# Kernel optimization log

Hardware: AMD Instinct MI355X
Metric: run time of the kernel (lower is better)

Reference implementation:

```python
import jax, jax.numpy as jnp
import numpy as np

# Flax nn.LSTMCell math: gates i,f,g,o; input dense has no bias, hidden dense has bias.
# We fuse the four gate projections into single [D,4H] / [H,4H] matrices in order (i,f,g,o).

def _lstm_layer(x, Wx, Wh, b):
    # x: [B,T,D], Wx: [D,4H], Wh: [H,4H], b: [4H]
    B = x.shape[0]
    H = Wh.shape[0]
    # Precompute input projections for the whole sequence (one big GEMM).
    xW = jnp.einsum('btd,dg->btg', x, Wx) + b  # [B,T,4H]

    def step(carry, xw_t):
        c, h = carry
        z = xw_t + h @ Wh  # [B,4H]
        i, f, g, o = jnp.split(z, 4, axis=-1)
        i = jax.nn.sigmoid(i)
        f = jax.nn.sigmoid(f)
        g = jnp.tanh(g)
        o = jax.nn.sigmoid(o)
        c = f * c + i * g
        h = o * jnp.tanh(c)
        return (c, h), h

    init = (jnp.zeros((B, H), x.dtype), jnp.zeros((B, H), x.dtype))
    _, ys = jax.lax.scan(step, init, jnp.swapaxes(xW, 0, 1))  # scan over T
    return jnp.swapaxes(ys, 0, 1)  # [B,T,H]


def setup_inputs() -> dict:
    key = jax.random.key(0)
    ks = jax.random.split(key, 7)
    B, T, D, H = 64, 512, 512, 1024
    s = lambda fan_in: 1.0 / np.sqrt(fan_in)
    x = jax.random.normal(ks[0], (B, T, D), dtype=jnp.float32)
    Wx0 = jax.random.normal(ks[1], (D, 4 * H), dtype=jnp.float32) * s(D)
    Wh0 = jax.random.normal(ks[2], (H, 4 * H), dtype=jnp.float32) * s(H)
    b0 = jnp.zeros((4 * H,), dtype=jnp.float32)
    Wx1 = jax.random.normal(ks[3], (H, 4 * H), dtype=jnp.float32) * s(H)
    Wh1 = jax.random.normal(ks[4], (H, 4 * H), dtype=jnp.float32) * s(H)
    b1 = jnp.zeros((4 * H,), dtype=jnp.float32)
    return {"x": x, "Wx0": Wx0, "Wh0": Wh0, "b0": b0, "Wx1": Wx1, "Wh1": Wh1, "b1": b1}


def reference(x, Wx0, Wh0, b0, Wx1, Wh1, b1):
    h1 = _lstm_layer(x, Wx0, Wh0, b0)
    h2 = _lstm_layer(h1, Wx1, Wh1, b1)
    return h2
```

## Files before the change

kernel.cpp:

```cpp
#include <hip/hip_runtime.h>

typedef __attribute__((ext_vector_type(8))) short short8;
typedef __attribute__((ext_vector_type(4))) float f32x4;

#define WS_XB     0ull
#define WS_W0T    33554432ull
#define WS_W1T    46137344ull
#define WS_RING0  62914560ull
#define WS_RING1  67108864ull
#define WS_BAR    71303168ull
#define SLOT_ELEMS 65536
#define SLOT_BYTES 131072

#define BAR_ARR(g)  ((g) * 16)
#define BAR_ROOT    256
#define BAR_REL(g)  (272 + (g) * 16)

__device__ __forceinline__ unsigned short f2bf(float f) {
  unsigned u = __float_as_uint(f);
  u += 0x7FFFu + ((u >> 16) & 1u);
  return (unsigned short)(u >> 16);
}

__device__ __forceinline__ float sigm(float x) { return 1.0f / (1.0f + __expf(-x)); }

__global__ void sentinel_kernel(float* out) { out[0] = 1.0e6f; }

__global__ void convert_x_kernel(const float* __restrict__ x, unsigned short* __restrict__ xb) {
  int i = blockIdx.x * 256 + threadIdx.x;
  const float4 v = ((const float4*)x)[i];
  unsigned long long pack = (unsigned long long)f2bf(v.x)
                          | ((unsigned long long)f2bf(v.y) << 16)
                          | ((unsigned long long)f2bf(v.z) << 32)
                          | ((unsigned long long)f2bf(v.w) << 48);
  ((unsigned long long*)xb)[i] = pack;
}

__global__ void transpose_weights_kernel(const float* __restrict__ wx, const float* __restrict__ wh,
                                         unsigned short* __restrict__ dst, int Kx, int Ktot) {
  __shared__ float tile[32][33];
  const int k0 = blockIdx.x * 32, n0 = blockIdx.y * 32;
  const int tx = threadIdx.x, ty = threadIdx.y;
#pragma unroll
  for (int i = 0; i < 4; ++i) {
    int k = k0 + ty + i * 8;
    tile[ty + i * 8][tx] = (k < Kx) ? wx[(size_t)k * 4096 + n0 + tx]
                                    : wh[(size_t)(k - Kx) * 4096 + n0 + tx];
  }
  __syncthreads();
#pragma unroll
  for (int i = 0; i < 4; ++i) {
    int n = n0 + ty + i * 8;
    int r = (n & 1023) * 4 + (n >> 10);
    dst[(size_t)r * Ktot + k0 + tx] = f2bf(tile[tx][ty + i * 8]);
  }
}

template<int N1, int NBLK>
__device__ __forceinline__ void lstm_step_mfma(int a0b, int a1b,
    const unsigned short* __restrict__ r1p, const unsigned short* __restrict__ r2p,
    f32x4& acc0, f32x4& acc1)
{
  extern __shared__ unsigned short lds[];
  short8 buf[4][8];

  auto loadB = [&](int slot, int blk) {
    const unsigned short* p = (blk < N1) ? (r1p + blk * 256) : (r2p + (blk - N1) * 256);
#pragma unroll
    for (int j = 0; j < 8; ++j) buf[slot][j] = *(const short8*)(p + j * 32);
  };
  auto compute8 = [&](int slot, int kg) {
#pragma unroll
    for (int j = 0; j < 8; ++j) {
      const int ko = kg + j * 32;
      short8 a0 = *(const short8*)&lds[a0b + ko];
      short8 a1 = *(const short8*)&lds[a1b + ko];
      acc0 = __builtin_amdgcn_mfma_f32_16x16x32_bf16(a0, buf[slot][j], acc0, 0, 0, 0);
      acc1 = __builtin_amdgcn_mfma_f32_16x16x32_bf16(a1, buf[slot][j], acc1, 0, 0, 0);
    }
  };

  loadB(0, 0); loadB(1, 1); loadB(2, 2); loadB(3, 3);
  __builtin_amdgcn_sched_barrier(0);
#pragma unroll
  for (int bp = 0; bp < NBLK; ++bp) {
    compute8(bp & 3, bp * 256);
    if (bp + 4 < NBLK) loadB(bp & 3, bp + 4);
    __builtin_amdgcn_sched_barrier(0);
  }
}

__global__ void __launch_bounds__(256, 1) lstm_persistent(
    const unsigned short* __restrict__ xb,
    const unsigned short* __restrict__ w0t,
    const unsigned short* __restrict__ w1t,
    const float* __restrict__ b0v, const float* __restrict__ b1v,
    unsigned short* __restrict__ ring0, unsigned short* __restrict__ ring1,
    unsigned* __restrict__ bar,
    float* __restrict__ out)
{
  extern __shared__ unsigned short lds[];

  const int wg    = blockIdx.x;
  const int group = wg >> 7;
  const int wgl   = wg & 127;
  const int hu0   = wgl * 8;
  const int tid   = threadIdx.x;
  const int lane  = tid & 63;
  const int wid   = tid >> 6;
  const int c16   = lane & 15;
  const int row4  = lane >> 4;
  const int bb    = wid * 16 + c16;

  const int K    = group ? 2048 : 1536;
  const int KPAD = group ? 2056 : 1544;

  {
    const unsigned short* wsrc = (group ? w1t : w0t) + (size_t)(wgl * 32) * K;
    const int kv = K >> 3;
    for (int c = tid; c < 32 * kv; c += 256) {
      int r = c / kv, q = c - r * kv;
      int srcr = 8 * ((r & 15) >> 2) + 4 * (r >> 4) + (r & 3);
      *(short8*)&lds[r * KPAD + q * 8] = *(const short8*)&wsrc[(size_t)srcr * K + q * 8];
    }
  }
  __syncthreads();

  const float* bsrc = group ? b1v : b0v;
  float bias0[4], bias1[4];
#pragma unroll
  for (int j = 0; j < 4; ++j) {
    bias0[j] = bsrc[j * 1024 + hu0 + 2 * row4];
    bias1[j] = bsrc[j * 1024 + hu0 + 2 * row4 + 1];
  }

  const int a0b = c16 * KPAD + 8 * row4;
  const int a1b = a0b + 16 * KPAD;

  const int lofs = (bb << 10) + 8 * row4;
  const unsigned short* x_cur = xb + ((size_t)bb << 18) + 8 * row4;
  unsigned* rwb = (unsigned*)(group ? ring1 : ring0) + (((bb << 10) + hu0) >> 1) + row4;
  float* out_base = out + ((size_t)bb << 19) + hu0 + 2 * row4;

  const int mygrp = wg >> 4;
  unsigned* grpc  = bar + BAR_ARR(mygrp);
  unsigned* rootc = bar + BAR_ROOT;
  unsigned* relc  = bar + BAR_REL(mygrp);

  float cst0 = 0.0f, cst1 = 0.0f;

  for (int s = 0; s <= 512; ++s) {
    const bool active = group ? (s >= 1) : (s < 512);
    if (active) {
      const int t = group ? (s - 1) : s;

      f32x4 acc0 = { bias0[0], bias0[1], bias0[2], bias0[3] };
      f32x4 acc1 = { bias1[0], bias1[1], bias1[2], bias1[3] };

      const unsigned short* h0rd = ring0 + ((s - 1) & 31) * SLOT_ELEMS + lofs;
      if (group == 0) {
        lstm_step_mfma<2, 6>(a0b, a1b, x_cur, h0rd, acc0, acc1);
        x_cur += 512;
      } else {
        const unsigned short* h1rd = ring1 + ((s - 2) & 31) * SLOT_ELEMS + lofs;
        lstm_step_mfma<4, 8>(a0b, a1b, h0rd, h1rd, acc0, acc1);
      }

      float hv0, hv1;
      {
        float iv = sigm(acc0[0]), fv = sigm(acc0[1]);
        float gv = tanhf(acc0[2]), ov = sigm(acc0[3]);
        cst0 = fv * cst0 + iv * gv;
        hv0 = ov * tanhf(cst0);
      }
      {
        float iv = sigm(acc1[0]), fv = sigm(acc1[1]);
        float gv = tanhf(acc1[2]), ov = sigm(acc1[3]);
        cst1 = fv * cst1 + iv * gv;
        hv1 = ov * tanhf(cst1);
      }
      unsigned hp = (unsigned)f2bf(hv0) | ((unsigned)f2bf(hv1) << 16);
      (void)__hip_atomic_exchange(rwb + (t & 31) * (SLOT_ELEMS / 2), hp,
                                  __ATOMIC_RELAXED, __HIP_MEMORY_SCOPE_AGENT);
      if (group) {
        float2 o2; o2.x = hv0; o2.y = hv1;
        *(float2*)(out_base + ((size_t)t << 10)) = o2;
      }
    }

    __syncthreads();
    if (tid == 0) {
      unsigned old = __hip_atomic_fetch_add(grpc, 1u, __ATOMIC_RELAXED, __HIP_MEMORY_SCOPE_AGENT);
      if (old == (unsigned)(16 * s + 15)) {
        unsigned old2 = __hip_atomic_fetch_add(rootc, 1u, __ATOMIC_RELAXED, __HIP_MEMORY_SCOPE_AGENT);
        if (old2 == (unsigned)(16 * s + 15)) {
#pragma unroll
          for (int g2 = 0; g2 < 16; ++g2)
            (void)__hip_atomic_exchange(bar + BAR_REL(g2), (unsigned)(s + 1),
                                        __ATOMIC_RELAXED, __HIP_MEMORY_SCOPE_AGENT);
        }
      }
      while (__hip_atomic_load(relc, __ATOMIC_RELAXED, __HIP_MEMORY_SCOPE_AGENT) < (unsigned)(s + 1))
        __builtin_amdgcn_s_sleep(1);
    }
    __syncthreads();
  }
}

extern "C" void kernel_launch(void* const* d_in, const int* in_sizes, int n_in,
                              void* d_out, int out_size, void* d_ws, size_t ws_size,
                              hipStream_t stream) {
  const float* x   = (const float*)d_in[0];
  const float* Wx0 = (const float*)d_in[1];
  const float* Wh0 = (const float*)d_in[2];
  const float* b0  = (const float*)d_in[3];
  const float* Wx1 = (const float*)d_in[4];
  const float* Wh1 = (const float*)d_in[5];
  const float* b1  = (const float*)d_in[6];
  float* outp = (float*)d_out;

  char* ws = (char*)d_ws;
  unsigned short* xbp   = (unsigned short*)(ws + WS_XB);
  unsigned short* w0tp  = (unsigned short*)(ws + WS_W0T);
  unsigned short* w1tp  = (unsigned short*)(ws + WS_W1T);
  unsigned short* ring0 = (unsigned short*)(ws + WS_RING0);
  unsigned short* ring1 = (unsigned short*)(ws + WS_RING1);
  unsigned*       barp  = (unsigned*)(ws + WS_BAR);

  sentinel_kernel<<<dim3(1), dim3(1), 0, stream>>>(outp);
  convert_x_kernel<<<dim3(16384), dim3(256), 0, stream>>>(x, xbp);
  transpose_weights_kernel<<<dim3(48, 128), dim3(32, 8), 0, stream>>>(Wx0, Wh0, w0tp, 512, 1536);
  transpose_weights_kernel<<<dim3(64, 128), dim3(32, 8), 0, stream>>>(Wx1, Wh1, w1tp, 1024, 2048);
  hipMemsetAsync(ring0 + 31 * SLOT_ELEMS, 0, SLOT_BYTES, stream);
  hipMemsetAsync(ring1 + 31 * SLOT_ELEMS, 0, SLOT_BYTES, stream);
  hipMemsetAsync(barp, 0, 4096, stream);

  void* kargs[] = { (void*)&xbp, (void*)&w0tp, (void*)&w1tp, (void*)&b0, (void*)&b1,
                    (void*)&ring0, (void*)&ring1, (void*)&barp, (void*)&outp };
  hipError_t e = hipLaunchCooperativeKernel((void*)lstm_persistent, dim3(256), dim3(256),
                                            kargs, 32 * 2056 * 2 , stream);
  if (e != hipSuccess) {
    lstm_persistent<<<dim3(256), dim3(256), 32 * 2056 * 2, stream>>>(
        xbp, w0tp, w1tp, b0, b1, ring0, ring1, barp, outp);
  }
}
```

Measured before the change: 5.195 ms.

## Replace hierarchical grid barrier with flat per-group counters and decoupled layer progress

Replaces the two-level arrive/root/release grid barrier with 16 flat per-group arrival counters that a whole wavefront polls at once with a ballot. Layer-0 blocks now wait only on layer-0 peers for the current step, plus a loose check that layer 1 is no more than about 30 steps behind so the ring is not overrun; layer-1 blocks wait on all groups. This removes the serialized release hop and lets layer 0 run ahead of layer 1. It also preloads all B fragments for a step into registers at once instead of a 4-deep rotating buffer, and shrinks the LDS row padding to 2 elements, which makes 16-byte LDS reads misaligned and may raise bank conflicts or register pressure.

```diff
diff --git a/kernel.cpp b/kernel.cpp
--- a/kernel.cpp
+++ b/kernel.cpp
@@ -12,10 +12,6 @@
 #define SLOT_ELEMS 65536
 #define SLOT_BYTES 131072
 
-#define BAR_ARR(g)  ((g) * 16)
-#define BAR_ROOT    256
-#define BAR_REL(g)  (272 + (g) * 16)
-
 __device__ __forceinline__ unsigned short f2bf(float f) {
   unsigned u = __float_as_uint(f);
   u += 0x7FFFu + ((u >> 16) & 1u);
@@ -62,31 +58,30 @@
     f32x4& acc0, f32x4& acc1)
 {
   extern __shared__ unsigned short lds[];
-  short8 buf[4][8];
-
-  auto loadB = [&](int slot, int blk) {
-    const unsigned short* p = (blk < N1) ? (r1p + blk * 256) : (r2p + (blk - N1) * 256);
-#pragma unroll
-    for (int j = 0; j < 8; ++j) buf[slot][j] = *(const short8*)(p + j * 32);
-  };
-  auto compute8 = [&](int slot, int kg) {
+  short8 buf[NBLK][8];
+
+#pragma unroll
+  for (int bp = 0; bp < NBLK; ++bp) {
+    const unsigned short* p = (bp < N1) ? (r1p + bp * 256) : (r2p + (bp - N1) * 256);
+#pragma unroll
+    for (int j = 0; j < 8; ++j) buf[bp][j] = *(const short8*)(p + j * 32);
+  }
+  __builtin_amdgcn_sched_barrier(0);
+
+#pragma unroll
+  for (int bp = 0; bp < NBLK; ++bp) {
+#pragma unroll
+    for (int j = 0; j < 8; ++j)
+      asm volatile("" :: "v"(buf[bp][j]));
+    __builtin_amdgcn_sched_barrier(0);
 #pragma unroll
     for (int j = 0; j < 8; ++j) {
-      const int ko = kg + j * 32;
+      const int ko = bp * 256 + j * 32;
       short8 a0 = *(const short8*)&lds[a0b + ko];
       short8 a1 = *(const short8*)&lds[a1b + ko];
-      acc0 = __builtin_amdgcn_mfma_f32_16x16x32_bf16(a0, buf[slot][j], acc0, 0, 0, 0);
-      acc1 = __builtin_amdgcn_mfma_f32_16x16x32_bf16(a1, buf[slot][j], acc1, 0, 0, 0);
-    }
-  };
-
-  loadB(0, 0); loadB(1, 1); loadB(2, 2); loadB(3, 3);
-  __builtin_amdgcn_sched_barrier(0);
-#pragma unroll
-  for (int bp = 0; bp < NBLK; ++bp) {
-    compute8(bp & 3, bp * 256);
-    if (bp + 4 < NBLK) loadB(bp & 3, bp + 4);
-    __builtin_amdgcn_sched_barrier(0);
+      acc0 = __builtin_amdgcn_mfma_f32_16x16x32_bf16(a0, buf[bp][j], acc0, 0, 0, 0);
+      acc1 = __builtin_amdgcn_mfma_f32_16x16x32_bf16(a1, buf[bp][j], acc1, 0, 0, 0);
+    }
   }
 }
 
@@ -113,7 +108,7 @@
   const int bb    = wid * 16 + c16;
 
   const int K    = group ? 2048 : 1536;
-  const int KPAD = group ? 2056 : 1544;
+  const int KPAD = group ? 2050 : 1538;
 
   {
     const unsigned short* wsrc = (group ? w1t : w0t) + (size_t)(wgl * 32) * K;
@@ -142,69 +137,70 @@
   unsigned* rwb = (unsigned*)(group ? ring1 : ring0) + (((bb << 10) + hu0) >> 1) + row4;
   float* out_base = out + ((size_t)bb << 19) + hu0 + 2 * row4;
 
-  const int mygrp = wg >> 4;
-  unsigned* grpc  = bar + BAR_ARR(mygrp);
-  unsigned* rootc = bar + BAR_ROOT;
-  unsigned* relc  = bar + BAR_REL(mygrp);
-
   float cst0 = 0.0f, cst1 = 0.0f;
 
-  for (int s = 0; s <= 512; ++s) {
-    const bool active = group ? (s >= 1) : (s < 512);
-    if (active) {
-      const int t = group ? (s - 1) : s;
-
-      f32x4 acc0 = { bias0[0], bias0[1], bias0[2], bias0[3] };
-      f32x4 acc1 = { bias1[0], bias1[1], bias1[2], bias1[3] };
-
-      const unsigned short* h0rd = ring0 + ((s - 1) & 31) * SLOT_ELEMS + lofs;
-      if (group == 0) {
-        lstm_step_mfma<2, 6>(a0b, a1b, x_cur, h0rd, acc0, acc1);
-        x_cur += 512;
-      } else {
-        const unsigned short* h1rd = ring1 + ((s - 2) & 31) * SLOT_ELEMS + lofs;
-        lstm_step_mfma<4, 8>(a0b, a1b, h0rd, h1rd, acc0, acc1);
-      }
-
-      float hv0, hv1;
-      {
-        float iv = sigm(acc0[0]), fv = sigm(acc0[1]);
-        float gv = tanhf(acc0[2]), ov = sigm(acc0[3]);
-        cst0 = fv * cst0 + iv * gv;
-        hv0 = ov * tanhf(cst0);
-      }
-      {
-        float iv = sigm(acc1[0]), fv = sigm(acc1[1]);
-        float gv = tanhf(acc1[2]), ov = sigm(acc1[3]);
-        cst1 = fv * cst1 + iv * gv;
-        hv1 = ov * tanhf(cst1);
-      }
-      unsigned hp = (unsigned)f2bf(hv0) | ((unsigned)f2bf(hv1) << 16);
-      (void)__hip_atomic_exchange(rwb + (t & 31) * (SLOT_ELEMS / 2), hp,
-                                  __ATOMIC_RELAXED, __HIP_MEMORY_SCOPE_AGENT);
-      if (group) {
-        float2 o2; o2.x = hv0; o2.y = hv1;
-        *(float2*)(out_base + ((size_t)t << 10)) = o2;
-      }
-    }
+  auto compute_episode = [&](int s) {
+    const int t = group ? (s - 1) : s;
+
+    f32x4 acc0 = { bias0[0], bias0[1], bias0[2], bias0[3] };
+    f32x4 acc1 = { bias1[0], bias1[1], bias1[2], bias1[3] };
+
+    const unsigned short* h0rd = ring0 + ((s - 1) & 31) * SLOT_ELEMS + lofs;
+    if (group == 0) {
+      lstm_step_mfma<2, 6>(a0b, a1b, x_cur, h0rd, acc0, acc1);
+      x_cur += 512;
+    } else {
+      const unsigned short* h1rd = ring1 + ((s - 2) & 31) * SLOT_ELEMS + lofs;
+      lstm_step_mfma<4, 8>(a0b, a1b, h0rd, h1rd, acc0, acc1);
+    }
+
+    float hv0, hv1;
+    {
+      float iv = sigm(acc0[0]), fv = sigm(acc0[1]);
+      float gv = tanhf(acc0[2]), ov = sigm(acc0[3]);
+      cst0 = fv * cst0 + iv * gv;
+      hv0 = ov * tanhf(cst0);
+    }
+    {
+      float iv = sigm(acc1[0]), fv = sigm(acc1[1]);
+      float gv = tanhf(acc1[2]), ov = sigm(acc1[3]);
+      cst1 = fv * cst1 + iv * gv;
+      hv1 = ov * tanhf(cst1);
+    }
+    unsigned hp = (unsigned)f2bf(hv0) | ((unsigned)f2bf(hv1) << 16);
+    (void)__hip_atomic_exchange(rwb + (t & 31) * (SLOT_ELEMS / 2), hp,
+                                __ATOMIC_RELAXED, __HIP_MEMORY_SCOPE_AGENT);
+    if (group) {
+      float2 o2; o2.x = hv0; o2.y = hv1;
+      *(float2*)(out_base + ((size_t)t << 10)) = o2;
+    }
+  };
+
+  for (int s = 0; s < 512; ++s) {
+    const bool active = group ? (s >= 1) : true;
+    if (active) compute_episode(s);
 
     __syncthreads();
-    if (tid == 0) {
-      unsigned old = __hip_atomic_fetch_add(grpc, 1u, __ATOMIC_RELAXED, __HIP_MEMORY_SCOPE_AGENT);
-      if (old == (unsigned)(16 * s + 15)) {
-        unsigned old2 = __hip_atomic_fetch_add(rootc, 1u, __ATOMIC_RELAXED, __HIP_MEMORY_SCOPE_AGENT);
-        if (old2 == (unsigned)(16 * s + 15)) {
-#pragma unroll
-          for (int g2 = 0; g2 < 16; ++g2)
-            (void)__hip_atomic_exchange(bar + BAR_REL(g2), (unsigned)(s + 1),
-                                        __ATOMIC_RELAXED, __HIP_MEMORY_SCOPE_AGENT);
+    if (wid == 0) {
+      if (lane == 0)
+        __hip_atomic_fetch_add(bar + (wg >> 4), 1u, __ATOMIC_RELAXED, __HIP_MEMORY_SCOPE_AGENT);
+      const bool last = (group == 0) && (s == 511);
+      if (!last) {
+        int tgt;
+        if (group == 0) tgt = (lane < 8) ? 16 * (s + 1) : 16 * (s - 29);
+        else            tgt = 16 * (s + 1);
+        for (;;) {
+          int v = (lane < 16)
+            ? (int)__hip_atomic_load(bar + lane, __ATOMIC_RELAXED, __HIP_MEMORY_SCOPE_AGENT)
+            : 0x7FFFFFFF;
+          if (__ballot(v >= tgt) == ~0ull) break;
+          __builtin_amdgcn_s_sleep(1);
         }
       }
-      while (__hip_atomic_load(relc, __ATOMIC_RELAXED, __HIP_MEMORY_SCOPE_AGENT) < (unsigned)(s + 1))
-        __builtin_amdgcn_s_sleep(1);
     }
     __syncthreads();
   }
+  if (group) compute_episode(512);
 }
 
 extern "C" void kernel_launch(void* const* d_in, const int* in_sizes, int n_in,
@@ -238,9 +234,9 @@
   void* kargs[] = { (void*)&xbp, (void*)&w0tp, (void*)&w1tp, (void*)&b0, (void*)&b1,
                     (void*)&ring0, (void*)&ring1, (void*)&barp, (void*)&outp };
   hipError_t e = hipLaunchCooperativeKernel((void*)lstm_persistent, dim3(256), dim3(256),
-                                            kargs, 32 * 2056 * 2 , stream);
+                                            kargs, 32 * 2050 * 2 , stream);
   if (e != hipSuccess) {
-    lstm_persistent<<<dim3(256), dim3(256), 32 * 2056 * 2, stream>>>(
+    lstm_persistent<<<dim3(256), dim3(256), 32 * 2050 * 2, stream>>>(
         xbp, w0tp, w1tp, b0, b1, ring0, ring1, barp, outp);
   }
 }
```

Measured after the change: 10.89 ms. 2.1x slower.

## Flatten grid barrier to single counter, unroll B prefetch, shrink LDS padding

Applied to the files above, without the earlier changes.

Replaces the two-level (group then root) atomic barrier with a single global counter that all 256 workgroups increment, after which the last arriver writes release flags for the 16 groups. This removes one serialized atomic round-trip per step at the cost of more contention on a single address. It also manually unrolls the 4-slot B-register prefetch pipeline into named arrays so the per-slot indexing is static. It changes the LDS row padding from 8 to 2 elements, which alters the bank-conflict pattern of the weight reads.

```diff
diff --git a/kernel.cpp b/kernel.cpp
--- a/kernel.cpp
+++ b/kernel.cpp
@@ -12,10 +12,6 @@
 #define SLOT_ELEMS 65536
 #define SLOT_BYTES 131072
 
-#define BAR_ARR(g)  ((g) * 16)
-#define BAR_ROOT    256
-#define BAR_REL(g)  (272 + (g) * 16)
-
 __device__ __forceinline__ unsigned short f2bf(float f) {
   unsigned u = __float_as_uint(f);
   u += 0x7FFFu + ((u >> 16) & 1u);
@@ -62,32 +58,35 @@
     f32x4& acc0, f32x4& acc1)
 {
   extern __shared__ unsigned short lds[];
-  short8 buf[4][8];
-
-  auto loadB = [&](int slot, int blk) {
-    const unsigned short* p = (blk < N1) ? (r1p + blk * 256) : (r2p + (blk - N1) * 256);
-#pragma unroll
-    for (int j = 0; j < 8; ++j) buf[slot][j] = *(const short8*)(p + j * 32);
+  short8 s0[8], s1[8], s2[8], s3[8];
+
+  auto ldp = [&](int blk) { return (blk < N1) ? (r1p + blk * 256) : (r2p + (blk - N1) * 256); };
+  auto issue = [&](short8* dst, int blk) {
+    const unsigned short* p = ldp(blk);
+#pragma unroll
+    for (int j = 0; j < 8; ++j) dst[j] = *(const short8*)(p + j * 32);
   };
-  auto compute8 = [&](int slot, int kg) {
+  auto compute8 = [&](const short8* b, int bp) {
 #pragma unroll
     for (int j = 0; j < 8; ++j) {
-      const int ko = kg + j * 32;
+      const int ko = bp * 256 + j * 32;
       short8 a0 = *(const short8*)&lds[a0b + ko];
       short8 a1 = *(const short8*)&lds[a1b + ko];
-      acc0 = __builtin_amdgcn_mfma_f32_16x16x32_bf16(a0, buf[slot][j], acc0, 0, 0, 0);
-      acc1 = __builtin_amdgcn_mfma_f32_16x16x32_bf16(a1, buf[slot][j], acc1, 0, 0, 0);
+      acc0 = __builtin_amdgcn_mfma_f32_16x16x32_bf16(a0, b[j], acc0, 0, 0, 0);
+      acc1 = __builtin_amdgcn_mfma_f32_16x16x32_bf16(a1, b[j], acc1, 0, 0, 0);
     }
   };
 
-  loadB(0, 0); loadB(1, 1); loadB(2, 2); loadB(3, 3);
+  issue(s0, 0); issue(s1, 1); issue(s2, 2); issue(s3, 3);
   __builtin_amdgcn_sched_barrier(0);
-#pragma unroll
-  for (int bp = 0; bp < NBLK; ++bp) {
-    compute8(bp & 3, bp * 256);
-    if (bp + 4 < NBLK) loadB(bp & 3, bp + 4);
-    __builtin_amdgcn_sched_barrier(0);
-  }
+  compute8(s0, 0); if (NBLK > 4) { issue(s0, 4); __builtin_amdgcn_sched_barrier(0); }
+  compute8(s1, 1); if (NBLK > 5) { issue(s1, 5); __builtin_amdgcn_sched_barrier(0); }
+  compute8(s2, 2); if (NBLK > 6) { issue(s2, 6); __builtin_amdgcn_sched_barrier(0); }
+  compute8(s3, 3); if (NBLK > 7) { issue(s3, 7); __builtin_amdgcn_sched_barrier(0); }
+  if (NBLK > 4) compute8(s0, 4);
+  if (NBLK > 5) compute8(s1, 5);
+  if (NBLK > 6) compute8(s2, 6);
+  if (NBLK > 7) compute8(s3, 7);
 }
 
 __global__ void __launch_bounds__(256, 1) lstm_persistent(
@@ -113,7 +112,7 @@
   const int bb    = wid * 16 + c16;
 
   const int K    = group ? 2048 : 1536;
-  const int KPAD = group ? 2056 : 1544;
+  const int KPAD = group ? 2050 : 1538;
 
   {
     const unsigned short* wsrc = (group ? w1t : w0t) + (size_t)(wgl * 32) * K;
@@ -142,10 +141,8 @@
   unsigned* rwb = (unsigned*)(group ? ring1 : ring0) + (((bb << 10) + hu0) >> 1) + row4;
   float* out_base = out + ((size_t)bb << 19) + hu0 + 2 * row4;
 
-  const int mygrp = wg >> 4;
-  unsigned* grpc  = bar + BAR_ARR(mygrp);
-  unsigned* rootc = bar + BAR_ROOT;
-  unsigned* relc  = bar + BAR_REL(mygrp);
+  unsigned* rootc = bar;
+  unsigned* relc  = bar + 16 + (wg >> 4) * 16;
 
   float cst0 = 0.0f, cst1 = 0.0f;
 
@@ -190,15 +187,12 @@
 
     __syncthreads();
     if (tid == 0) {
-      unsigned old = __hip_atomic_fetch_add(grpc, 1u, __ATOMIC_RELAXED, __HIP_MEMORY_SCOPE_AGENT);
-      if (old == (unsigned)(16 * s + 15)) {
-        unsigned old2 = __hip_atomic_fetch_add(rootc, 1u, __ATOMIC_RELAXED, __HIP_MEMORY_SCOPE_AGENT);
-        if (old2 == (unsigned)(16 * s + 15)) {
-#pragma unroll
-          for (int g2 = 0; g2 < 16; ++g2)
-            (void)__hip_atomic_exchange(bar + BAR_REL(g2), (unsigned)(s + 1),
-                                        __ATOMIC_RELAXED, __HIP_MEMORY_SCOPE_AGENT);
-        }
+      unsigned old = __hip_atomic_fetch_add(rootc, 1u, __ATOMIC_RELAXED, __HIP_MEMORY_SCOPE_AGENT);
+      if (old == 256u * (unsigned)(s + 1) - 1u) {
+#pragma unroll
+        for (int g2 = 0; g2 < 16; ++g2)
+          (void)__hip_atomic_exchange(bar + 16 + g2 * 16, (unsigned)(s + 1),
+                                      __ATOMIC_RELAXED, __HIP_MEMORY_SCOPE_AGENT);
       }
       while (__hip_atomic_load(relc, __ATOMIC_RELAXED, __HIP_MEMORY_SCOPE_AGENT) < (unsigned)(s + 1))
         __builtin_amdgcn_s_sleep(1);
@@ -238,9 +232,9 @@
   void* kargs[] = { (void*)&xbp, (void*)&w0tp, (void*)&w1tp, (void*)&b0, (void*)&b1,
                     (void*)&ring0, (void*)&ring1, (void*)&barp, (void*)&outp };
   hipError_t e = hipLaunchCooperativeKernel((void*)lstm_persistent, dim3(256), dim3(256),
-                                            kargs, 32 * 2056 * 2 , stream);
+                                            kargs, 32 * 2050 * 2 , stream);
   if (e != hipSuccess) {
-    lstm_persistent<<<dim3(256), dim3(256), 32 * 2056 * 2, stream>>>(
+    lstm_persistent<<<dim3(256), dim3(256), 32 * 2050 * 2, stream>>>(
         xbp, w0tp, w1tp, b0, b1, ring0, ring1, barp, outp);
   }
 }
```

Result: slower. 10.31 ms (+98.5%).

## Split grid barrier per layer with cross-layer mirror flags and packed h stores

Applied to the files above, without the earlier changes.

Replaces the single 256-workgroup barrier with two per-layer barriers (8 sub-groups each). Each layer also waits on a mirror flag from the other layer: layer 0 may run up to 16 steps ahead of layer 1 within the 32-slot ring, while layer 1 waits for layer 0's current step. This is meant to decouple the layers and shorten the critical path of each barrier. It also packs two lanes' hidden outputs into one 64-bit atomic store via a shuffle and drops the sched_barriers in the MFMA loop. The risks are ring-slot reuse hazards and visibility ordering, since all atomics are relaxed.

```diff
diff --git a/kernel.cpp b/kernel.cpp
--- a/kernel.cpp
+++ b/kernel.cpp
@@ -12,9 +12,14 @@
 #define SLOT_ELEMS 65536
 #define SLOT_BYTES 131072
 
-#define BAR_ARR(g)  ((g) * 16)
-#define BAR_ROOT    256
-#define BAR_REL(g)  (272 + (g) * 16)
+#define ARR0(g)  ((g) * 16)
+#define ARR1(g)  (128 + (g) * 16)
+#define ROOT0    256
+#define ROOT1    272
+#define REL0(g)  (288 + (g) * 16)
+#define REL1(g)  (416 + (g) * 16)
+#define MIR0(g)  (544 + (g) * 16)
+#define MIR1(g)  (672 + (g) * 16)
 
 __device__ __forceinline__ unsigned short f2bf(float f) {
   unsigned u = __float_as_uint(f);
@@ -81,12 +86,10 @@
   };
 
   loadB(0, 0); loadB(1, 1); loadB(2, 2); loadB(3, 3);
-  __builtin_amdgcn_sched_barrier(0);
 #pragma unroll
   for (int bp = 0; bp < NBLK; ++bp) {
     compute8(bp & 3, bp * 256);
     if (bp + 4 < NBLK) loadB(bp & 3, bp + 4);
-    __builtin_amdgcn_sched_barrier(0);
   }
 }
 
@@ -139,72 +142,89 @@
 
   const int lofs = (bb << 10) + 8 * row4;
   const unsigned short* x_cur = xb + ((size_t)bb << 18) + 8 * row4;
-  unsigned* rwb = (unsigned*)(group ? ring1 : ring0) + (((bb << 10) + hu0) >> 1) + row4;
+  unsigned* rwb0 = (unsigned*)(group ? ring1 : ring0) + (((bb << 10) + hu0) >> 1);
   float* out_base = out + ((size_t)bb << 19) + hu0 + 2 * row4;
 
-  const int mygrp = wg >> 4;
-  unsigned* grpc  = bar + BAR_ARR(mygrp);
-  unsigned* rootc = bar + BAR_ROOT;
-  unsigned* relc  = bar + BAR_REL(mygrp);
+  const int grp = wgl >> 4;
+  unsigned* arrw = bar + (group ? ARR1(grp) : ARR0(grp));
+  unsigned* rootw = bar + (group ? ROOT1 : ROOT0);
+  unsigned* relw = bar + (group ? REL1(grp) : REL0(grp));
+  unsigned* mirw = bar + (group ? MIR0(grp) : MIR1(grp));
 
   float cst0 = 0.0f, cst1 = 0.0f;
 
-  for (int s = 0; s <= 512; ++s) {
-    const bool active = group ? (s >= 1) : (s < 512);
-    if (active) {
-      const int t = group ? (s - 1) : s;
-
-      f32x4 acc0 = { bias0[0], bias0[1], bias0[2], bias0[3] };
-      f32x4 acc1 = { bias1[0], bias1[1], bias1[2], bias1[3] };
-
-      const unsigned short* h0rd = ring0 + ((s - 1) & 31) * SLOT_ELEMS + lofs;
-      if (group == 0) {
-        lstm_step_mfma<2, 6>(a0b, a1b, x_cur, h0rd, acc0, acc1);
-        x_cur += 512;
-      } else {
-        const unsigned short* h1rd = ring1 + ((s - 2) & 31) * SLOT_ELEMS + lofs;
-        lstm_step_mfma<4, 8>(a0b, a1b, h0rd, h1rd, acc0, acc1);
-      }
-
-      float hv0, hv1;
-      {
-        float iv = sigm(acc0[0]), fv = sigm(acc0[1]);
-        float gv = tanhf(acc0[2]), ov = sigm(acc0[3]);
-        cst0 = fv * cst0 + iv * gv;
-        hv0 = ov * tanhf(cst0);
-      }
-      {
-        float iv = sigm(acc1[0]), fv = sigm(acc1[1]);
-        float gv = tanhf(acc1[2]), ov = sigm(acc1[3]);
-        cst1 = fv * cst1 + iv * gv;
-        hv1 = ov * tanhf(cst1);
-      }
-      unsigned hp = (unsigned)f2bf(hv0) | ((unsigned)f2bf(hv1) << 16);
-      (void)__hip_atomic_exchange(rwb + (t & 31) * (SLOT_ELEMS / 2), hp,
-                                  __ATOMIC_RELAXED, __HIP_MEMORY_SCOPE_AGENT);
-      if (group) {
-        float2 o2; o2.x = hv0; o2.y = hv1;
-        *(float2*)(out_base + ((size_t)t << 10)) = o2;
-      }
-    }
+  auto compute_episode = [&](int s) {
+    const int t = group ? (s - 1) : s;
+
+    f32x4 acc0 = { bias0[0], bias0[1], bias0[2], bias0[3] };
+    f32x4 acc1 = { bias1[0], bias1[1], bias1[2], bias1[3] };
+
+    const unsigned short* h0rd = ring0 + ((s - 1) & 31) * SLOT_ELEMS + lofs;
+    if (group == 0) {
+      lstm_step_mfma<2, 6>(a0b, a1b, x_cur, h0rd, acc0, acc1);
+      x_cur += 512;
+    } else {
+      const unsigned short* h1rd = ring1 + ((s - 2) & 31) * SLOT_ELEMS + lofs;
+      lstm_step_mfma<4, 8>(a0b, a1b, h0rd, h1rd, acc0, acc1);
+    }
+
+    float hv0, hv1;
+    {
+      float iv = sigm(acc0[0]), fv = sigm(acc0[1]);
+      float gv = tanhf(acc0[2]), ov = sigm(acc0[3]);
+      cst0 = fv * cst0 + iv * gv;
+      hv0 = ov * tanhf(cst0);
+    }
+    {
+      float iv = sigm(acc1[0]), fv = sigm(acc1[1]);
+      float gv = tanhf(acc1[2]), ov = sigm(acc1[3]);
+      cst1 = fv * cst1 + iv * gv;
+      hv1 = ov * tanhf(cst1);
+    }
+    unsigned hp  = (unsigned)f2bf(hv0) | ((unsigned)f2bf(hv1) << 16);
+    unsigned hpo = __shfl_down(hp, 16);
+    if ((row4 & 1) == 0) {
+      unsigned long long pk = (unsigned long long)hp | ((unsigned long long)hpo << 32);
+      unsigned long long* dst = (unsigned long long*)(rwb0 + (t & 31) * (SLOT_ELEMS / 2) + row4);
+      (void)__hip_atomic_exchange(dst, pk, __ATOMIC_RELAXED, __HIP_MEMORY_SCOPE_AGENT);
+    }
+    if (group) {
+      float2 o2; o2.x = hv0; o2.y = hv1;
+      *(float2*)(out_base + ((size_t)t << 10)) = o2;
+    }
+  };
+
+  for (int s = 0; s < 512; ++s) {
+    const bool active = group ? (s >= 1) : true;
+    if (active) compute_episode(s);
 
     __syncthreads();
     if (tid == 0) {
-      unsigned old = __hip_atomic_fetch_add(grpc, 1u, __ATOMIC_RELAXED, __HIP_MEMORY_SCOPE_AGENT);
+      unsigned old = __hip_atomic_fetch_add(arrw, 1u, __ATOMIC_RELAXED, __HIP_MEMORY_SCOPE_AGENT);
       if (old == (unsigned)(16 * s + 15)) {
-        unsigned old2 = __hip_atomic_fetch_add(rootc, 1u, __ATOMIC_RELAXED, __HIP_MEMORY_SCOPE_AGENT);
-        if (old2 == (unsigned)(16 * s + 15)) {
-#pragma unroll
-          for (int g2 = 0; g2 < 16; ++g2)
-            (void)__hip_atomic_exchange(bar + BAR_REL(g2), (unsigned)(s + 1),
+        unsigned old2 = __hip_atomic_fetch_add(rootw, 1u, __ATOMIC_RELAXED, __HIP_MEMORY_SCOPE_AGENT);
+        if (old2 == (unsigned)(8 * s + 7)) {
+#pragma unroll
+          for (int g2 = 0; g2 < 8; ++g2) {
+            (void)__hip_atomic_exchange(bar + (group ? REL1(g2) : REL0(g2)), (unsigned)(s + 1),
                                         __ATOMIC_RELAXED, __HIP_MEMORY_SCOPE_AGENT);
+            (void)__hip_atomic_exchange(bar + (group ? MIR1(g2) : MIR0(g2)), (unsigned)(s + 1),
+                                        __ATOMIC_RELAXED, __HIP_MEMORY_SCOPE_AGENT);
+          }
         }
       }
-      while (__hip_atomic_load(relc, __ATOMIC_RELAXED, __HIP_MEMORY_SCOPE_AGENT) < (unsigned)(s + 1))
+      const int own_tgt = s + 1;
+      const int mir_tgt = group ? (s + 1) : (s - 15);
+      for (;;) {
+        int a = (int)__hip_atomic_load(relw, __ATOMIC_RELAXED, __HIP_MEMORY_SCOPE_AGENT);
+        int b = (int)__hip_atomic_load(mirw, __ATOMIC_RELAXED, __HIP_MEMORY_SCOPE_AGENT);
+        if (a >= own_tgt && b >= mir_tgt) break;
         __builtin_amdgcn_s_sleep(1);
+      }
     }
     __syncthreads();
   }
+  if (group) compute_episode(512);
 }
 
 extern "C" void kernel_launch(void* const* d_in, const int* in_sizes, int n_in,
```

New measurement: 5.897 ms. 13.5% more time.
